# Optimization experiments

Hardware: AMD Instinct MI355X
Metric: run time of the kernel (lower is better)

Reference implementation:

```python
import jax, jax.numpy as jnp
import numpy as np

D_MODEL = 1024
N_HEADS = 16
D_K = D_MODEL // N_HEADS
B, T = 2, 2048


def setup_inputs() -> dict:
    key = jax.random.key(0)
    ks = jax.random.split(key, 9)
    s = 1.0 / np.sqrt(D_MODEL)
    def lin(kw, kb):
        W = jax.random.uniform(kw, (D_MODEL, D_MODEL), jnp.float32, -s, s)
        b = jax.random.uniform(kb, (D_MODEL,), jnp.float32, -s, s)
        return W, b
    Wq, bq = lin(ks[0], ks[1])
    Wk, bk = lin(ks[2], ks[3])
    Wv, bv = lin(ks[4], ks[5])
    Wo, bo = lin(ks[6], ks[7])
    x = jax.random.normal(ks[8], (B, T, D_MODEL), jnp.float32)
    return {"x": x, "Wq": Wq, "bq": bq, "Wk": Wk, "bk": bk,
            "Wv": Wv, "bv": bv, "Wo": Wo, "bo": bo}


def reference(x, Wq, bq, Wk, bk, Wv, bv, Wo, bo):
    Bn, Tn, _ = x.shape
    # torch Linear: x @ W.T + b
    def proj(W, b):
        y = x @ W.T + b  # [B, T, D]
        return y.reshape(Bn, Tn, N_HEADS, D_K).transpose(0, 2, 1, 3)  # [B, H, T, d_k]
    q = proj(Wq, bq)
    k = proj(Wk, bk)
    v = proj(Wv, bv)
    scores = jnp.einsum('bhqd,bhkd->bhqk', q, k) / jnp.sqrt(jnp.float32(D_K))
    causal = jnp.tril(jnp.ones((Tn, Tn), dtype=bool))  # True = keep
    scores = jnp.where(causal[None, None], scores, -jnp.inf)
    attn = jax.nn.softmax(scores, axis=-1)
    # dropout is identity in eval mode
    ctx = jnp.einsum('bhqk,bhkd->bhqd', attn, v)
    ctx = ctx.transpose(0, 2, 1, 3).reshape(Bn, Tn, D_MODEL)
    return ctx @ Wo.T + bo
```

## Files before the change

### kernel.cpp

```cpp
#include <hip/hip_runtime.h>
#include <hip/hip_bf16.h>
#include <stdint.h>

#define D_MODEL 1024
#define NH 16
#define DK 64
#define BB 2
#define TT 2048
#define NROWS (BB*TT)

#define QSCALE 0.180336880f

typedef short bf16x8 __attribute__((ext_vector_type(8)));
typedef short bf16x4 __attribute__((ext_vector_type(4)));
typedef float f32x4  __attribute__((ext_vector_type(4)));

#if __has_builtin(__builtin_amdgcn_mfma_f32_16x16x16_bf16)
  #define MFMA16(a,b,c) __builtin_amdgcn_mfma_f32_16x16x16_bf16(a,b,c,0,0,0)
  #define HAVE_M16 1
#elif __has_builtin(__builtin_amdgcn_mfma_f32_16x16x16bf16_1k)
  #define MFMA16(a,b,c) __builtin_amdgcn_mfma_f32_16x16x16bf16_1k(a,b,c,0,0,0)
  #define HAVE_M16 1
#else
  #define HAVE_M16 0
#endif

#if __has_builtin(__builtin_amdgcn_global_load_lds)
  #define HAVE_GLDS 1
__device__ __forceinline__ void gload16(const unsigned short* g, unsigned short* lds){
    __builtin_amdgcn_global_load_lds(
        (const __attribute__((address_space(1))) unsigned int*)g,
        (__attribute__((address_space(3))) unsigned int*)lds, 16, 0, 0);
}
#else
  #define HAVE_GLDS 0
#endif

__device__ __forceinline__ float fexp2(float x){
#if __has_builtin(__builtin_amdgcn_exp2f)
    return __builtin_amdgcn_exp2f(x);
#else
    return exp2f(x);
#endif
}

__device__ __forceinline__ unsigned pkbf(float a, float b){
    float2 t; t.x = a; t.y = b;
    __hip_bfloat162 h = __float22bfloat162_rn(t);
    return *reinterpret_cast<unsigned*>(&h);
}
__device__ __forceinline__ unsigned short bfbits(float a){
    __hip_bfloat16 h = __float2bfloat16(a);
    return *reinterpret_cast<unsigned short*>(&h);
}

__global__ __launch_bounds__(256) void conv_all(
    const float* __restrict__ x,
    const float* __restrict__ Wq, const float* __restrict__ Wk,
    const float* __restrict__ Wv, const float* __restrict__ Wo,
    unsigned short* __restrict__ xb, unsigned short* __restrict__ wb)
{
    const int blk = blockIdx.x;
    const float* src; unsigned short* dst; size_t i;
    if (blk < 2048) {
        src = x; dst = xb;
        i = ((size_t)blk * 256 + threadIdx.x) * 8;
    } else {
        const int t = (blk - 2048) >> 9;
        src = (t == 0) ? Wq : (t == 1) ? Wk : (t == 2) ? Wv : Wo;
        dst = wb + (size_t)t * D_MODEL * D_MODEL;
        i = ((size_t)((blk - 2048) & 511) * 256 + threadIdx.x) * 8;
    }
    float4 a = *(const float4*)(src + i);
    float4 b = *(const float4*)(src + i + 4);
    uint4 w;
    w.x = pkbf(a.x, a.y); w.y = pkbf(a.z, a.w);
    w.z = pkbf(b.x, b.y); w.w = pkbf(b.z, b.w);
    *(uint4*)(dst + i) = w;
}

__global__ __launch_bounds__(256) void conv_bf16(
    const float* __restrict__ x, unsigned short* __restrict__ y)
{
    size_t i = ((size_t)blockIdx.x * 256 + threadIdx.x) * 8;
    float4 a = *(const float4*)(x + i);
    float4 b = *(const float4*)(x + i + 4);
    uint4 w;
    w.x = pkbf(a.x, a.y); w.y = pkbf(a.z, a.w);
    w.z = pkbf(b.x, b.y); w.w = pkbf(b.z, b.w);
    *(uint4*)(y + i) = w;
}

#if HAVE_GLDS
template<int MI, int NB, bool CF32>
__device__ __forceinline__ void gemm_async(
    const unsigned short* __restrict__ Ap, const unsigned short* __restrict__ Bp,
    const float* __restrict__ bias, void* __restrict__ Cp,
    bool vt, float scale, unsigned short* As, unsigned short* Bs)
{
    constexpr int BMt = MI * 32, BNt = NB * 32;
    const int K = D_MODEL, N = D_MODEL;
    const int tid  = threadIdx.x;
    const int m0   = blockIdx.y * BMt;
    const int n0   = blockIdx.x * BNt;
    const int lane = tid & 63;
    const int w    = tid >> 6;
    const int wm   = (w >> 1) * (MI * 16);
    const int wn   = (w &  1) * (BNt / 2);
    const int l16  = lane & 15;
    const int quad = lane >> 4;
    const int crow = lane >> 2;
    const int ccol = (lane & 3) * 8;

    constexpr int CA = MI / 2;
    constexpr int CB = NB / 2;

    auto issue = [&](int buf, int k0){
        #pragma unroll
        for (int c = 0; c < CA; ++c) {
            const int chunk = w * CA + c;
            gload16(Ap + (size_t)(m0 + chunk*16 + crow) * K + k0 + ccol,
                    As + buf * BMt * 32 + chunk * 512);
        }
        #pragma unroll
        for (int c = 0; c < CB; ++c) {
            const int chunk = w * CB + c;
            gload16(Bp + (size_t)(n0 + chunk*16 + crow) * K + k0 + ccol,
                    Bs + buf * BNt * 32 + chunk * 512);
        }
    };

    f32x4 acc[MI][NB] = {};
    issue(0, 0);

    constexpr int ITER = D_MODEL / 32;
    for (int it = 0; it < ITER; ++it) {
        __syncthreads();
        if (it + 1 < ITER) issue((it + 1) & 1, (it + 1) * 32);
        const unsigned short* A = As + (it & 1) * BMt * 32;
        const unsigned short* B = Bs + (it & 1) * BNt * 32;
        bf16x8 af[MI], bg[NB];
        #pragma unroll
        for (int i = 0; i < MI; ++i)
            af[i] = *(const bf16x8*)&A[(wm + 16*i + l16) * 32 + quad * 8];
        #pragma unroll
        for (int j = 0; j < NB; ++j)
            bg[j] = *(const bf16x8*)&B[(wn + 16*j + l16) * 32 + quad * 8];
        #pragma unroll
        for (int i = 0; i < MI; ++i)
            #pragma unroll
            for (int j = 0; j < NB; ++j)
                acc[i][j] = __builtin_amdgcn_mfma_f32_16x16x32_bf16(af[i], bg[j], acc[i][j], 0, 0, 0);
    }

    #pragma unroll
    for (int j = 0; j < NB; ++j) {
        const int n = n0 + wn + 16*j + l16;
        const float bj = bias[n];
        #pragma unroll
        for (int i = 0; i < MI; ++i) {
            const int m = m0 + wm + 16*i + quad*4;
            if (vt) {
                const int b = m >> 11, t = m & 2047;
                ushort4 wv;
                wv.x = bfbits(acc[i][j][0] + bj);
                wv.y = bfbits(acc[i][j][1] + bj);
                wv.z = bfbits(acc[i][j][2] + bj);
                wv.w = bfbits(acc[i][j][3] + bj);
                *(ushort4*)((unsigned short*)Cp + (size_t)b * D_MODEL * TT
                            + (size_t)n * TT + t) = wv;
            } else {
                #pragma unroll
                for (int r = 0; r < 4; ++r) {
                    float v = (acc[i][j][r] + bj) * scale;
                    if (CF32) ((float*)Cp)[(size_t)(m + r) * N + n] = v;
                    else      ((__hip_bfloat16*)Cp)[(size_t)(m + r) * N + n] = __float2bfloat16(v);
                }
            }
        }
    }
}
#endif

#define ASTR 40

template<int MI, int NB, bool AF32, bool BF32, bool CF32>
__device__ __forceinline__ void gemm_body(
    const void* __restrict__ Ap, const void* __restrict__ Bp,
    const float* __restrict__ bias, void* __restrict__ Cp,
    bool vt, float scale, unsigned short* As, unsigned short* Bs)
{
    constexpr int BMt = MI * 32, BNt = NB * 32;
    const int K = D_MODEL, N = D_MODEL;
    const int tid  = threadIdx.x;
    const int m0   = blockIdx.y * BMt;
    const int n0   = blockIdx.x * BNt;
    const int lane = tid & 63;
    const int wave = tid >> 6;
    const int wm   = (wave >> 1) * (MI * 16);
    const int wn   = (wave &  1) * (BNt / 2);
    const int l16  = lane & 15;
    const int quad = lane >> 4;
    const int ar = (MI == 4) ? (tid >> 1) : (tid >> 2);
    const int ac = (MI == 4) ? ((tid & 1) * 16) : ((tid & 3) * 8);
    const int br = (NB == 4) ? (tid >> 1) : (tid >> 2);
    const int bc = (NB == 4) ? ((tid & 1) * 16) : ((tid & 3) * 8);

    uint4 pa[4], pb[4];

    auto loadA = [&](int k0){
        if (AF32) {
            const float* p = (const float*)Ap + (size_t)(m0 + ar) * K + k0 + ac;
            pa[0] = *(const uint4*)(p);     pa[1] = *(const uint4*)(p + 4);
            if (MI == 4) { pa[2] = *(const uint4*)(p + 8); pa[3] = *(const uint4*)(p + 12); }
        } else {
            const unsigned short* p = (const unsigned short*)Ap + (size_t)(m0 + ar) * K + k0 + ac;
            pa[0] = *(const uint4*)(p);
            if (MI == 4) pa[1] = *(const uint4*)(p + 8);
        }
    };
    auto loadB = [&](int k0){
        if (BF32) {
            const float* p = (const float*)Bp + (size_t)(n0 + br) * K + k0 + bc;
            pb[0] = *(const uint4*)(p); pb[1] = *(const uint4*)(p + 4);
            if (NB == 4) { pb[2] = *(const uint4*)(p + 8); pb[3] = *(const uint4*)(p + 12); }
        } else {
            const unsigned short* p = (const unsigned short*)Bp + (size_t)(n0 + br) * K + k0 + bc;
            pb[0] = *(const uint4*)(p);
            if (NB == 4) pb[1] = *(const uint4*)(p + 8);
        }
    };
    auto stage = [&](int buf){
        unsigned short* A = As + buf * BMt * ASTR;
        unsigned short* B = Bs + buf * BNt * ASTR;
        if (AF32) {
            const float* f = (const float*)pa;
            uint4 w0;
            w0.x = pkbf(f[0], f[1]); w0.y = pkbf(f[2], f[3]);
            w0.z = pkbf(f[4], f[5]); w0.w = pkbf(f[6], f[7]);
            *(uint4*)&A[ar*ASTR + ac] = w0;
            if (MI == 4) {
                uint4 w1;
                w1.x = pkbf(f[8], f[9]);   w1.y = pkbf(f[10], f[11]);
                w1.z = pkbf(f[12], f[13]); w1.w = pkbf(f[14], f[15]);
                *(uint4*)&A[ar*ASTR + ac + 8] = w1;
            }
        } else {
            *(uint4*)&A[ar*ASTR + ac] = pa[0];
            if (MI == 4) *(uint4*)&A[ar*ASTR + ac + 8] = pa[1];
        }
        if (BF32) {
            const float* g = (const float*)pb;
            uint4 v0;
            v0.x = pkbf(g[0], g[1]); v0.y = pkbf(g[2], g[3]);
            v0.z = pkbf(g[4], g[5]); v0.w = pkbf(g[6], g[7]);
            *(uint4*)&B[br*ASTR + bc] = v0;
            if (NB == 4) {
                uint4 v1;
                v1.x = pkbf(g[8], g[9]);   v1.y = pkbf(g[10], g[11]);
                v1.z = pkbf(g[12], g[13]); v1.w = pkbf(g[14], g[15]);
                *(uint4*)&B[br*ASTR + bc + 8] = v1;
            }
        } else {
            *(uint4*)&B[br*ASTR + bc] = pb[0];
            if (NB == 4) *(uint4*)&B[br*ASTR + bc + 8] = pb[1];
        }
    };

    f32x4 acc[MI][NB] = {};
    loadA(0); loadB(0);
    stage(0);

    constexpr int ITER = D_MODEL / 32;
    for (int it = 0; it < ITER; ++it) {
        __syncthreads();
        if (it + 1 < ITER) { loadA((it + 1) * 32); loadB((it + 1) * 32); }
        const unsigned short* A = As + (it & 1) * BMt * ASTR;
        const unsigned short* B = Bs + (it & 1) * BNt * ASTR;
        bf16x8 af[MI], bg[NB];
        #pragma unroll
        for (int i = 0; i < MI; ++i)
            af[i] = *(const bf16x8*)&A[(wm + 16*i + l16) * ASTR + quad * 8];
        #pragma unroll
        for (int j = 0; j < NB; ++j)
            bg[j] = *(const bf16x8*)&B[(wn + 16*j + l16) * ASTR + quad * 8];
        #pragma unroll
        for (int i = 0; i < MI; ++i)
            #pragma unroll
            for (int j = 0; j < NB; ++j)
                acc[i][j] = __builtin_amdgcn_mfma_f32_16x16x32_bf16(af[i], bg[j], acc[i][j], 0, 0, 0);
        if (it + 1 < ITER) stage((it + 1) & 1);
    }

    #pragma unroll
    for (int j = 0; j < NB; ++j) {
        const int n = n0 + wn + 16*j + l16;
        const float bj = bias[n];
        #pragma unroll
        for (int i = 0; i < MI; ++i) {
            const int m = m0 + wm + 16*i + quad*4;
            if (vt) {
                const int b = m >> 11, t = m & 2047;
                ushort4 wv;
                wv.x = bfbits(acc[i][j][0] + bj);
                wv.y = bfbits(acc[i][j][1] + bj);
                wv.z = bfbits(acc[i][j][2] + bj);
                wv.w = bfbits(acc[i][j][3] + bj);
                *(ushort4*)((unsigned short*)Cp + (size_t)b * D_MODEL * TT
                            + (size_t)n * TT + t) = wv;
            } else {
                #pragma unroll
                for (int r = 0; r < 4; ++r) {
                    float v = (acc[i][j][r] + bj) * scale;
                    if (CF32) ((float*)Cp)[(size_t)(m + r) * N + n] = v;
                    else      ((__hip_bfloat16*)Cp)[(size_t)(m + r) * N + n] = __float2bfloat16(v);
                }
            }
        }
    }
}

template<bool AF32, bool BF32>
__device__ __forceinline__ void qkv_sel(
    const void* x,
    const void* Wq, const float* bq, const void* Wk, const float* bk,
    const void* Wv, const float* bv,
    __hip_bfloat16* Qw, __hip_bfloat16* Kd, __hip_bfloat16* Vd,
    unsigned short* As, unsigned short* Bs)
{
    const void* W; const float* bi; void* C; bool vt = false; float sc = 1.0f;
    if      (blockIdx.z == 0) { W = Wq; bi = bq; C = Qw; sc = QSCALE; }
    else if (blockIdx.z == 1) { W = Wk; bi = bk; C = Kd; }
    else                      { W = Wv; bi = bv; C = Vd; vt = true; }
    gemm_body<4, 4, AF32, BF32, false>(x, W, bi, C, vt, sc, As, Bs);
}

#define QKV_KERNEL(name, AF, BF, XT)                                          \
__global__ __launch_bounds__(256, 3) void name(                               \
    const XT* __restrict__ x,                                                 \
    const void* __restrict__ Wq, const float* __restrict__ bq,                \
    const void* __restrict__ Wk, const float* __restrict__ bk,                \
    const void* __restrict__ Wv, const float* __restrict__ bv,                \
    __hip_bfloat16* __restrict__ Qw, __hip_bfloat16* __restrict__ Kd,         \
    __hip_bfloat16* __restrict__ Vd)                                          \
{                                                                             \
    __shared__ __align__(16) unsigned short As[2*128*ASTR];                   \
    __shared__ __align__(16) unsigned short Bs[2*128*ASTR];                   \
    qkv_sel<AF, BF>(x, Wq, bq, Wk, bk, Wv, bv, Qw, Kd, Vd, As, Bs);           \
}
QKV_KERNEL(gemm_qkv_f32, true,  true,  float)
QKV_KERNEL(gemm_qkv_xb,  false, true,  unsigned short)

__global__ __launch_bounds__(256, 3) void gemm_qkv_bb(
    const unsigned short* __restrict__ x,
    const unsigned short* __restrict__ Wq, const float* __restrict__ bq,
    const unsigned short* __restrict__ Wk, const float* __restrict__ bk,
    const unsigned short* __restrict__ Wv, const float* __restrict__ bv,
    __hip_bfloat16* __restrict__ Qw, __hip_bfloat16* __restrict__ Kd,
    __hip_bfloat16* __restrict__ Vd)
{
#if HAVE_GLDS
    __shared__ __align__(16) unsigned short As[2*128*32];
    __shared__ __align__(16) unsigned short Bs[2*128*32];
    const unsigned short* W; const float* bi; void* C; bool vt = false; float sc = 1.0f;
    if      (blockIdx.z == 0) { W = Wq; bi = bq; C = Qw; sc = QSCALE; }
    else if (blockIdx.z == 1) { W = Wk; bi = bk; C = Kd; }
    else                      { W = Wv; bi = bv; C = Vd; vt = true; }
    gemm_async<4, 4, false>(x, W, bi, C, vt, sc, As, Bs);
#else
    __shared__ __align__(16) unsigned short As[2*128*ASTR];
    __shared__ __align__(16) unsigned short Bs[2*128*ASTR];
    qkv_sel<false, false>(x, Wq, bq, Wk, bk, Wv, bv, Qw, Kd, Vd, As, Bs);
#endif
}

__global__ __launch_bounds__(256, 2) void gemm_out_f(
    const __hip_bfloat16* __restrict__ ctx, const void* __restrict__ Wo,
    const float* __restrict__ bo, float* __restrict__ out)
{
    __shared__ __align__(16) unsigned short As[2*128*ASTR];
    __shared__ __align__(16) unsigned short Bs[2*64*ASTR];
    gemm_body<4, 2, false, true, true>(ctx, Wo, bo, out, false, 1.0f, As, Bs);
}

__global__ __launch_bounds__(256, 2) void gemm_out_b(
    const __hip_bfloat16* __restrict__ ctx, const unsigned short* __restrict__ Wo,
    const float* __restrict__ bo, float* __restrict__ out)
{
#if HAVE_GLDS
    __shared__ __align__(16) unsigned short As[2*128*32];
    __shared__ __align__(16) unsigned short Bs[2*64*32];
    gemm_async<4, 2, true>((const unsigned short*)ctx, Wo, bo, out, false, 1.0f, As, Bs);
#else
    __shared__ __align__(16) unsigned short As[2*128*ASTR];
    __shared__ __align__(16) unsigned short Bs[2*64*ASTR];
    gemm_body<4, 2, false, false, true>(ctx, Wo, bo, out, false, 1.0f, As, Bs);
#endif
}

#define QSTR 68

__global__ __launch_bounds__(256, 4) void attn_mfma(
    const __hip_bfloat16* __restrict__ Q,
    const __hip_bfloat16* __restrict__ Km,
    const __hip_bfloat16* __restrict__ Vt,
    __hip_bfloat16* __restrict__ ctx)
{
    __shared__ __align__(16) unsigned short Ks [2][64*QSTR];
    __shared__ __align__(16) unsigned short VTs[2][64*QSTR];
#if !HAVE_M16
    __shared__ __align__(16) unsigned short QP[64*QSTR];
#endif

    const int tid = threadIdx.x;
    const int blk = blockIdx.x;
    const int i4 = blk & 255;
    const int j4 = blk >> 8;
    const int qt = (j4 & 1) ? (i4 & 31) : 31 - (i4 & 31);
    const int bh = (i4 >> 5) + (j4 << 3);
    const int b  = bh >> 4;
    const int h  = bh & 15;
    const int q0  = qt << 6;
    const size_t rowbase = (size_t)b * TT;
    const int colbase = h * DK;

    const int lane = tid & 63;
    const int w    = tid >> 6;
    const int l16  = lane & 15;
    const int quad = lane >> 4;
    const int lr = tid >> 2;
    const int lc = (tid & 3) << 4;

    const unsigned short* Vtb = (const unsigned short*)Vt + (size_t)b * D_MODEL * TT;

    uint4 kr0, kr1, vt0, vt1;
    auto prefetch = [&](int kv0){
        const unsigned short* pk = (const unsigned short*)Km +
            (rowbase + kv0 + lr) * D_MODEL + colbase + lc;
        kr0 = *(const uint4*)(pk);
        kr1 = *(const uint4*)(pk + 8);
        const unsigned short* pv = Vtb + (size_t)(colbase + lr) * TT + kv0 + lc;
        vt0 = *(const uint4*)(pv);
        vt1 = *(const uint4*)(pv + 8);
    };
    auto stageKV = [&](int buf){
        *(uint4*)&Ks [buf][lr*QSTR + lc]     = kr0;
        *(uint4*)&Ks [buf][lr*QSTR + lc + 8] = kr1;
        *(uint4*)&VTs[buf][lr*QSTR + lc]     = vt0;
        *(uint4*)&VTs[buf][lr*QSTR + lc + 8] = vt1;
    };

#if HAVE_M16
    const unsigned short* qp = (const unsigned short*)Q +
        (rowbase + q0 + 16*w + l16) * D_MODEL + colbase + quad*8;
    bf16x8 af_q0 = *(const bf16x8*)(qp);
    bf16x8 af_q1 = *(const bf16x8*)(qp + 32);

    prefetch(0);
    stageKV(0);

    f32x4 o[4] = {};
    float lpart = 0.0f;

    for (int kt = 0; kt <= qt; ++kt) {
        __syncthreads();
        if (kt < qt) prefetch((kt + 1) << 6);
        const int cur = kt & 1;

        f32x4 s[4] = {};
        #pragma unroll
        for (int cb = 0; cb < 4; ++cb) {
            bf16x8 ak0 = *(const bf16x8*)&Ks[cur][(16*cb + l16)*QSTR + quad*8];
            bf16x8 ak1 = *(const bf16x8*)&Ks[cur][(16*cb + l16)*QSTR + quad*8 + 32];
            s[cb] = __builtin_amdgcn_mfma_f32_16x16x32_bf16(ak0, af_q0, s[cb], 0, 0, 0);
            s[cb] = __builtin_amdgcn_mfma_f32_16x16x32_bf16(ak1, af_q1, s[cb], 0, 0, 0);
        }

        bf16x4 bp[4];
        if (kt < qt) {
            #pragma unroll
            for (int cb = 0; cb < 4; ++cb) {
                float p[4];
                #pragma unroll
                for (int r = 0; r < 4; ++r) {
                    p[r] = fexp2(fminf(s[cb][r], 36.0f));
                    lpart += p[r];
                }
                uint2 u; u.x = pkbf(p[0], p[1]); u.y = pkbf(p[2], p[3]);
                bp[cb] = *reinterpret_cast<bf16x4*>(&u);
            }
        } else {
            #pragma unroll
            for (int cb = 0; cb < 4; ++cb) {
                float p[4];
                #pragma unroll
                for (int r = 0; r < 4; ++r) {
                    float v = fminf(s[cb][r], 36.0f);
                    bool keep = (16*cb + quad*4 + r <= 16*w + l16);
                    p[r] = keep ? fexp2(v) : 0.0f;
                    lpart += p[r];
                }
                uint2 u; u.x = pkbf(p[0], p[1]); u.y = pkbf(p[2], p[3]);
                bp[cb] = *reinterpret_cast<bf16x4*>(&u);
            }
        }

        #pragma unroll
        for (int nb = 0; nb < 4; ++nb)
            #pragma unroll
            for (int cb = 0; cb < 4; ++cb) {
                bf16x4 av = *(const bf16x4*)&VTs[cur][(16*nb + l16)*QSTR + 16*cb + quad*4];
                o[nb] = MFMA16(av, bp[cb], o[nb]);
            }

        if (kt < qt) stageKV((kt + 1) & 1);
    }

    lpart += __shfl_xor(lpart, 16);
    lpart += __shfl_xor(lpart, 32);
    const float inv_l = 1.0f / lpart;

    {
        const size_t row = (rowbase + q0 + 16*w + l16) * (size_t)D_MODEL + colbase;
        #pragma unroll
        for (int nb = 0; nb < 4; ++nb) {
            ushort4 wv;
            wv.x = bfbits(o[nb][0] * inv_l);
            wv.y = bfbits(o[nb][1] * inv_l);
            wv.z = bfbits(o[nb][2] * inv_l);
            wv.w = bfbits(o[nb][3] * inv_l);
            *(ushort4*)((unsigned short*)ctx + row + 16*nb + quad*4) = wv;
        }
    }
#else
    {
        const unsigned short* p = (const unsigned short*)Q +
            (rowbase + q0 + lr) * D_MODEL + colbase + lc;
        *(uint4*)&QP[lr*QSTR + lc]     = *(const uint4*)(p);
        *(uint4*)&QP[lr*QSTR + lc + 8] = *(const uint4*)(p + 8);
    }
    prefetch(0);
    __syncthreads();
    bf16x8 af_q0 = *(const bf16x8*)&QP[(16*w + l16)*QSTR + quad*8];
    bf16x8 af_q1 = *(const bf16x8*)&QP[(16*w + l16)*QSTR + quad*8 + 32];
    stageKV(0);

    const short ob = (short)0x3F80;
    bf16x8 ones = { ob, ob, ob, ob, ob, ob, ob, ob };
    f32x4 o[4] = {};
    f32x4 l_acc = {};

    for (int kt = 0; kt <= qt; ++kt) {
        __syncthreads();
        if (kt < qt) prefetch((kt + 1) << 6);
        const int cur = kt & 1;

        f32x4 s[4] = {};
        #pragma unroll
        for (int cb = 0; cb < 4; ++cb) {
            bf16x8 bk0 = *(const bf16x8*)&Ks[cur][(16*cb + l16)*QSTR + quad*8];
            bf16x8 bk1 = *(const bf16x8*)&Ks[cur][(16*cb + l16)*QSTR + quad*8 + 32];
            s[cb] = __builtin_amdgcn_mfma_f32_16x16x32_bf16(af_q0, bk0, s[cb], 0, 0, 0);
            s[cb] = __builtin_amdgcn_mfma_f32_16x16x32_bf16(af_q1, bk1, s[cb], 0, 0, 0);
        }
        const bool diag = (kt == qt);
        #pragma unroll
        for (int cb = 0; cb < 4; ++cb)
            #pragma unroll
            for (int r = 0; r < 4; ++r) {
                float v = fminf(s[cb][r], 36.0f);
                float p = (diag && (16*cb + l16 > 16*w + quad*4 + r)) ? 0.0f : fexp2(v);
                QP[(16*w + quad*4 + r)*QSTR + 16*cb + l16] = bfbits(p);
            }
        bf16x8 ap0 = *(const bf16x8*)&QP[(16*w + l16)*QSTR + quad*8];
        bf16x8 ap1 = *(const bf16x8*)&QP[(16*w + l16)*QSTR + quad*8 + 32];
        #pragma unroll
        for (int nb = 0; nb < 4; ++nb) {
            bf16x8 bv0 = *(const bf16x8*)&VTs[cur][(16*nb + l16)*QSTR + quad*8];
            bf16x8 bv1 = *(const bf16x8*)&VTs[cur][(16*nb + l16)*QSTR + quad*8 + 32];
            o[nb] = __builtin_amdgcn_mfma_f32_16x16x32_bf16(ap0, bv0, o[nb], 0, 0, 0);
            o[nb] = __builtin_amdgcn_mfma_f32_16x16x32_bf16(ap1, bv1, o[nb], 0, 0, 0);
        }
        l_acc = __builtin_amdgcn_mfma_f32_16x16x32_bf16(ap0, ones, l_acc, 0, 0, 0);
        l_acc = __builtin_amdgcn_mfma_f32_16x16x32_bf16(ap1, ones, l_acc, 0, 0, 0);
        if (kt < qt) stageKV((kt + 1) & 1);
    }
    float inv_l[4];
    #pragma unroll
    for (int r = 0; r < 4; ++r) inv_l[r] = 1.0f / l_acc[r];
    #pragma unroll
    for (int nb = 0; nb < 4; ++nb)
        #pragma unroll
        for (int r = 0; r < 4; ++r) {
            const int row = q0 + 16*w + quad*4 + r;
            ctx[(rowbase + row)*D_MODEL + colbase + 16*nb + l16] =
                __float2bfloat16(o[nb][r] * inv_l[r]);
        }
#endif
}

extern "C" void kernel_launch(void* const* d_in, const int* in_sizes, int n_in,
                              void* d_out, int out_size, void* d_ws, size_t ws_size,
                              hipStream_t stream) {
    const float* x  = (const float*)d_in[0];
    const float* Wq = (const float*)d_in[1];
    const float* bq = (const float*)d_in[2];
    const float* Wk = (const float*)d_in[3];
    const float* bk = (const float*)d_in[4];
    const float* Wv = (const float*)d_in[5];
    const float* bv = (const float*)d_in[6];
    const float* Wo = (const float*)d_in[7];
    const float* bo = (const float*)d_in[8];

    __hip_bfloat16* Qw = (__hip_bfloat16*)d_ws;
    __hip_bfloat16* Kd = (__hip_bfloat16*)d_out;
    __hip_bfloat16* Vd = Kd + (size_t)NROWS * D_MODEL;
    unsigned short* xb = (unsigned short*)d_ws + (size_t)NROWS * D_MODEL;
    unsigned short* wb = xb + (size_t)NROWS * D_MODEL;
    const size_t WSZ = (size_t)D_MODEL * D_MODEL;

    dim3 gqkv(D_MODEL / 128, NROWS / 128, 3);
    dim3 gout(D_MODEL / 64, NROWS / 128);
    const bool haveXB = ws_size >= (size_t)(16u << 20);
    const bool haveWB = ws_size >= (size_t)(24u << 20);

    if (haveWB) {
        conv_all<<<4096, 256, 0, stream>>>(x, Wq, Wk, Wv, Wo, xb, wb);
        gemm_qkv_bb<<<gqkv, 256, 0, stream>>>(xb, wb, bq, wb + WSZ, bk,
                                              wb + 2*WSZ, bv, Qw, Kd, Vd);
    } else if (haveXB) {
        conv_bf16<<<(NROWS * D_MODEL) / (256 * 8), 256, 0, stream>>>(x, xb);
        gemm_qkv_xb<<<gqkv, 256, 0, stream>>>(xb, Wq, bq, Wk, bk, Wv, bv, Qw, Kd, Vd);
    } else {
        gemm_qkv_f32<<<gqkv, 256, 0, stream>>>(x, Wq, bq, Wk, bk, Wv, bv, Qw, Kd, Vd);
    }

    attn_mfma<<<BB * NH * (TT / 64), 256, 0, stream>>>(Qw, Kd, Vd, Qw);

    if (haveWB)
        gemm_out_b<<<gout, 256, 0, stream>>>(Qw, wb + 3*WSZ, bo, (float*)d_out);
    else
        gemm_out_f<<<gout, 256, 0, stream>>>(Qw, Wo, bo, (float*)d_out);
}
```

Measured before the change: 188.5 us.

## Pair low and high causal query tiles per attention block to share K/V loads

```diff
diff --git a/kernel.cpp b/kernel.cpp
--- a/kernel.cpp
+++ b/kernel.cpp
@@ -400,7 +400,7 @@
 
 #define QSTR 68
 
-__global__ __launch_bounds__(256, 4) void attn_mfma(
+__global__ __launch_bounds__(256, 2) void attn_mfma(
     const __hip_bfloat16* __restrict__ Q,
     const __hip_bfloat16* __restrict__ Km,
     const __hip_bfloat16* __restrict__ Vt,
@@ -416,11 +416,13 @@
     const int blk = blockIdx.x;
     const int i4 = blk & 255;
     const int j4 = blk >> 8;
-    const int qt = (j4 & 1) ? (i4 & 31) : 31 - (i4 & 31);
-    const int bh = (i4 >> 5) + (j4 << 3);
+    const int ql = (j4 & 1) ? 15 - (i4 & 15) : (i4 & 15);
+    const int qh = 31 - ql;
+    const int bh = (i4 >> 4) + (j4 << 4);
     const int b  = bh >> 4;
     const int h  = bh & 15;
-    const int q0  = qt << 6;
+    const int q0l = ql << 6;
+    const int q0h = qh << 6;
     const size_t rowbase = (size_t)b * TT;
     const int colbase = h * DK;
 
@@ -451,77 +453,104 @@
     };
 
 #if HAVE_M16
-    const unsigned short* qp = (const unsigned short*)Q +
-        (rowbase + q0 + 16*w + l16) * D_MODEL + colbase + quad*8;
-    bf16x8 af_q0 = *(const bf16x8*)(qp);
-    bf16x8 af_q1 = *(const bf16x8*)(qp + 32);
+    const unsigned short* qpl = (const unsigned short*)Q +
+        (rowbase + q0l + 16*w + l16) * D_MODEL + colbase + quad*8;
+    bf16x8 af_ql0 = *(const bf16x8*)(qpl);
+    bf16x8 af_ql1 = *(const bf16x8*)(qpl + 32);
+    const unsigned short* qph = (const unsigned short*)Q +
+        (rowbase + q0h + 16*w + l16) * D_MODEL + colbase + quad*8;
+    bf16x8 af_qh0 = *(const bf16x8*)(qph);
+    bf16x8 af_qh1 = *(const bf16x8*)(qph + 32);
 
     prefetch(0);
     stageKV(0);
 
-    f32x4 o[4] = {};
-    float lpart = 0.0f;
-
-    for (int kt = 0; kt <= qt; ++kt) {
+    f32x4 ol[4] = {}, oh[4] = {};
+    float lpl = 0.0f, lph = 0.0f;
+
+    auto softmax_t = [&](f32x4* s, bf16x4* bp, float& lp, bool diag){
+        #pragma unroll
+        for (int cb = 0; cb < 4; ++cb) {
+            float p[4];
+            #pragma unroll
+            for (int r = 0; r < 4; ++r) {
+                float v = fminf(s[cb][r], 36.0f);
+                bool keep = !diag || (16*cb + quad*4 + r <= 16*w + l16);
+                p[r] = keep ? fexp2(v) : 0.0f;
+                lp += p[r];
+            }
+            uint2 u; u.x = pkbf(p[0], p[1]); u.y = pkbf(p[2], p[3]);
+            bp[cb] = *reinterpret_cast<bf16x4*>(&u);
+        }
+    };
+
+    for (int kt = 0; kt <= ql; ++kt) {
         __syncthreads();
-        if (kt < qt) prefetch((kt + 1) << 6);
+        prefetch((kt + 1) << 6);
         const int cur = kt & 1;
 
-        f32x4 s[4] = {};
+        f32x4 sl[4] = {}, sh[4] = {};
         #pragma unroll
         for (int cb = 0; cb < 4; ++cb) {
             bf16x8 ak0 = *(const bf16x8*)&Ks[cur][(16*cb + l16)*QSTR + quad*8];
             bf16x8 ak1 = *(const bf16x8*)&Ks[cur][(16*cb + l16)*QSTR + quad*8 + 32];
-            s[cb] = __builtin_amdgcn_mfma_f32_16x16x32_bf16(ak0, af_q0, s[cb], 0, 0, 0);
-            s[cb] = __builtin_amdgcn_mfma_f32_16x16x32_bf16(ak1, af_q1, s[cb], 0, 0, 0);
-        }
-
-        bf16x4 bp[4];
-        if (kt < qt) {
-            #pragma unroll
-            for (int cb = 0; cb < 4; ++cb) {
-                float p[4];
-                #pragma unroll
-                for (int r = 0; r < 4; ++r) {
-                    p[r] = fexp2(fminf(s[cb][r], 36.0f));
-                    lpart += p[r];
-                }
-                uint2 u; u.x = pkbf(p[0], p[1]); u.y = pkbf(p[2], p[3]);
-                bp[cb] = *reinterpret_cast<bf16x4*>(&u);
-            }
-        } else {
-            #pragma unroll
-            for (int cb = 0; cb < 4; ++cb) {
-                float p[4];
-                #pragma unroll
-                for (int r = 0; r < 4; ++r) {
-                    float v = fminf(s[cb][r], 36.0f);
-                    bool keep = (16*cb + quad*4 + r <= 16*w + l16);
-                    p[r] = keep ? fexp2(v) : 0.0f;
-                    lpart += p[r];
-                }
-                uint2 u; u.x = pkbf(p[0], p[1]); u.y = pkbf(p[2], p[3]);
-                bp[cb] = *reinterpret_cast<bf16x4*>(&u);
-            }
-        }
+            sl[cb] = __builtin_amdgcn_mfma_f32_16x16x32_bf16(ak0, af_ql0, sl[cb], 0, 0, 0);
+            sl[cb] = __builtin_amdgcn_mfma_f32_16x16x32_bf16(ak1, af_ql1, sl[cb], 0, 0, 0);
+            sh[cb] = __builtin_amdgcn_mfma_f32_16x16x32_bf16(ak0, af_qh0, sh[cb], 0, 0, 0);
+            sh[cb] = __builtin_amdgcn_mfma_f32_16x16x32_bf16(ak1, af_qh1, sh[cb], 0, 0, 0);
+        }
+
+        bf16x4 bpl[4], bph[4];
+        if (kt == ql) softmax_t(sl, bpl, lpl, true);
+        else          softmax_t(sl, bpl, lpl, false);
+        softmax_t(sh, bph, lph, false);
 
         #pragma unroll
         for (int nb = 0; nb < 4; ++nb)
             #pragma unroll
             for (int cb = 0; cb < 4; ++cb) {
                 bf16x4 av = *(const bf16x4*)&VTs[cur][(16*nb + l16)*QSTR + 16*cb + quad*4];
-                o[nb] = MFMA16(av, bp[cb], o[nb]);
-            }
-
-        if (kt < qt) stageKV((kt + 1) & 1);
-    }
-
-    lpart += __shfl_xor(lpart, 16);
-    lpart += __shfl_xor(lpart, 32);
-    const float inv_l = 1.0f / lpart;
-
-    {
-        const size_t row = (rowbase + q0 + 16*w + l16) * (size_t)D_MODEL + colbase;
+                ol[nb] = MFMA16(av, bpl[cb], ol[nb]);
+                oh[nb] = MFMA16(av, bph[cb], oh[nb]);
+            }
+
+        stageKV((kt + 1) & 1);
+    }
+
+    for (int kt = ql + 1; kt <= qh; ++kt) {
+        __syncthreads();
+        if (kt < qh) prefetch((kt + 1) << 6);
+        const int cur = kt & 1;
+
+        f32x4 sh[4] = {};
+        #pragma unroll
+        for (int cb = 0; cb < 4; ++cb) {
+            bf16x8 ak0 = *(const bf16x8*)&Ks[cur][(16*cb + l16)*QSTR + quad*8];
+            bf16x8 ak1 = *(const bf16x8*)&Ks[cur][(16*cb + l16)*QSTR + quad*8 + 32];
+            sh[cb] = __builtin_amdgcn_mfma_f32_16x16x32_bf16(ak0, af_qh0, sh[cb], 0, 0, 0);
+            sh[cb] = __builtin_amdgcn_mfma_f32_16x16x32_bf16(ak1, af_qh1, sh[cb], 0, 0, 0);
+        }
+
+        bf16x4 bph[4];
+        if (kt == qh) softmax_t(sh, bph, lph, true);
+        else          softmax_t(sh, bph, lph, false);
+
+        #pragma unroll
+        for (int nb = 0; nb < 4; ++nb)
+            #pragma unroll
+            for (int cb = 0; cb < 4; ++cb) {
+                bf16x4 av = *(const bf16x4*)&VTs[cur][(16*nb + l16)*QSTR + 16*cb + quad*4];
+                oh[nb] = MFMA16(av, bph[cb], oh[nb]);
+            }
+
+        if (kt < qh) stageKV((kt + 1) & 1);
+    }
+
+    auto finish = [&](f32x4* o, float lp, int q0t){
+        lp += __shfl_xor(lp, 16);
+        lp += __shfl_xor(lp, 32);
+        const float inv_l = 1.0f / lp;
+        const size_t row = (rowbase + q0t + 16*w + l16) * (size_t)D_MODEL + colbase;
         #pragma unroll
         for (int nb = 0; nb < 4; ++nb) {
             ushort4 wv;
@@ -531,71 +560,80 @@
             wv.w = bfbits(o[nb][3] * inv_l);
             *(ushort4*)((unsigned short*)ctx + row + 16*nb + quad*4) = wv;
         }
-    }
+    };
+    finish(ol, lpl, q0l);
+    finish(oh, lph, q0h);
 #else
-    {
-        const unsigned short* p = (const unsigned short*)Q +
-            (rowbase + q0 + lr) * D_MODEL + colbase + lc;
-        *(uint4*)&QP[lr*QSTR + lc]     = *(const uint4*)(p);
-        *(uint4*)&QP[lr*QSTR + lc + 8] = *(const uint4*)(p + 8);
-    }
-    prefetch(0);
-    __syncthreads();
-    bf16x8 af_q0 = *(const bf16x8*)&QP[(16*w + l16)*QSTR + quad*8];
-    bf16x8 af_q1 = *(const bf16x8*)&QP[(16*w + l16)*QSTR + quad*8 + 32];
-    stageKV(0);
-
     const short ob = (short)0x3F80;
     bf16x8 ones = { ob, ob, ob, ob, ob, ob, ob, ob };
-    f32x4 o[4] = {};
-    f32x4 l_acc = {};
-
-    for (int kt = 0; kt <= qt; ++kt) {
+
+    for (int sel = 0; sel < 2; ++sel) {
+        const int qt = sel ? qh : ql;
+        const int q0 = qt << 6;
+
         __syncthreads();
-        if (kt < qt) prefetch((kt + 1) << 6);
-        const int cur = kt & 1;
-
-        f32x4 s[4] = {};
-        #pragma unroll
-        for (int cb = 0; cb < 4; ++cb) {
-            bf16x8 bk0 = *(const bf16x8*)&Ks[cur][(16*cb + l16)*QSTR + quad*8];
-            bf16x8 bk1 = *(const bf16x8*)&Ks[cur][(16*cb + l16)*QSTR + quad*8 + 32];
-            s[cb] = __builtin_amdgcn_mfma_f32_16x16x32_bf16(af_q0, bk0, s[cb], 0, 0, 0);
-            s[cb] = __builtin_amdgcn_mfma_f32_16x16x32_bf16(af_q1, bk1, s[cb], 0, 0, 0);
-        }
-        const bool diag = (kt == qt);
-        #pragma unroll
-        for (int cb = 0; cb < 4; ++cb)
+        {
+            const unsigned short* p = (const unsigned short*)Q +
+                (rowbase + q0 + lr) * D_MODEL + colbase + lc;
+            *(uint4*)&QP[lr*QSTR + lc]     = *(const uint4*)(p);
+            *(uint4*)&QP[lr*QSTR + lc + 8] = *(const uint4*)(p + 8);
+        }
+        prefetch(0);
+        __syncthreads();
+        bf16x8 af_q0 = *(const bf16x8*)&QP[(16*w + l16)*QSTR + quad*8];
+        bf16x8 af_q1 = *(const bf16x8*)&QP[(16*w + l16)*QSTR + quad*8 + 32];
+        stageKV(0);
+
+        f32x4 o[4] = {};
+        f32x4 l_acc = {};
+
+        for (int kt = 0; kt <= qt; ++kt) {
+            __syncthreads();
+            if (kt < qt) prefetch((kt + 1) << 6);
+            const int cur = kt & 1;
+
+            f32x4 s[4] = {};
+            #pragma unroll
+            for (int cb = 0; cb < 4; ++cb) {
+                bf16x8 bk0 = *(const bf16x8*)&Ks[cur][(16*cb + l16)*QSTR + quad*8];
+                bf16x8 bk1 = *(const bf16x8*)&Ks[cur][(16*cb + l16)*QSTR + quad*8 + 32];
+                s[cb] = __builtin_amdgcn_mfma_f32_16x16x32_bf16(af_q0, bk0, s[cb], 0, 0, 0);
+                s[cb] = __builtin_amdgcn_mfma_f32_16x16x32_bf16(af_q1, bk1, s[cb], 0, 0, 0);
+            }
+            const bool diag = (kt == qt);
+            #pragma unroll
+            for (int cb = 0; cb < 4; ++cb)
+                #pragma unroll
+                for (int r = 0; r < 4; ++r) {
+                    float v = fminf(s[cb][r], 36.0f);
+                    float p = (diag && (16*cb + l16 > 16*w + quad*4 + r)) ? 0.0f : fexp2(v);
+                    QP[(16*w + quad*4 + r)*QSTR + 16*cb + l16] = bfbits(p);
+                }
+            bf16x8 ap0 = *(const bf16x8*)&QP[(16*w + l16)*QSTR + quad*8];
+            bf16x8 ap1 = *(const bf16x8*)&QP[(16*w + l16)*QSTR + quad*8 + 32];
+            #pragma unroll
+            for (int nb = 0; nb < 4; ++nb) {
+                bf16x8 bv0 = *(const bf16x8*)&VTs[cur][(16*nb + l16)*QSTR + quad*8];
+                bf16x8 bv1 = *(const bf16x8*)&VTs[cur][(16*nb + l16)*QSTR + quad*8 + 32];
+                o[nb] = __builtin_amdgcn_mfma_f32_16x16x32_bf16(ap0, bv0, o[nb], 0, 0, 0);
+                o[nb] = __builtin_amdgcn_mfma_f32_16x16x32_bf16(ap1, bv1, o[nb], 0, 0, 0);
+            }
+            l_acc = __builtin_amdgcn_mfma_f32_16x16x32_bf16(ap0, ones, l_acc, 0, 0, 0);
+            l_acc = __builtin_amdgcn_mfma_f32_16x16x32_bf16(ap1, ones, l_acc, 0, 0, 0);
+            if (kt < qt) stageKV((kt + 1) & 1);
+        }
+        float inv_l[4];
+        #pragma unroll
+        for (int r = 0; r < 4; ++r) inv_l[r] = 1.0f / l_acc[r];
+        #pragma unroll
+        for (int nb = 0; nb < 4; ++nb)
             #pragma unroll
             for (int r = 0; r < 4; ++r) {
-                float v = fminf(s[cb][r], 36.0f);
-                float p = (diag && (16*cb + l16 > 16*w + quad*4 + r)) ? 0.0f : fexp2(v);
-                QP[(16*w + quad*4 + r)*QSTR + 16*cb + l16] = bfbits(p);
-            }
-        bf16x8 ap0 = *(const bf16x8*)&QP[(16*w + l16)*QSTR + quad*8];
-        bf16x8 ap1 = *(const bf16x8*)&QP[(16*w + l16)*QSTR + quad*8 + 32];
-        #pragma unroll
-        for (int nb = 0; nb < 4; ++nb) {
-            bf16x8 bv0 = *(const bf16x8*)&VTs[cur][(16*nb + l16)*QSTR + quad*8];
-            bf16x8 bv1 = *(const bf16x8*)&VTs[cur][(16*nb + l16)*QSTR + quad*8 + 32];
-            o[nb] = __builtin_amdgcn_mfma_f32_16x16x32_bf16(ap0, bv0, o[nb], 0, 0, 0);
-            o[nb] = __builtin_amdgcn_mfma_f32_16x16x32_bf16(ap1, bv1, o[nb], 0, 0, 0);
-        }
-        l_acc = __builtin_amdgcn_mfma_f32_16x16x32_bf16(ap0, ones, l_acc, 0, 0, 0);
-        l_acc = __builtin_amdgcn_mfma_f32_16x16x32_bf16(ap1, ones, l_acc, 0, 0, 0);
-        if (kt < qt) stageKV((kt + 1) & 1);
-    }
-    float inv_l[4];
-    #pragma unroll
-    for (int r = 0; r < 4; ++r) inv_l[r] = 1.0f / l_acc[r];
-    #pragma unroll
-    for (int nb = 0; nb < 4; ++nb)
-        #pragma unroll
-        for (int r = 0; r < 4; ++r) {
-            const int row = q0 + 16*w + quad*4 + r;
-            ctx[(rowbase + row)*D_MODEL + colbase + 16*nb + l16] =
-                __float2bfloat16(o[nb][r] * inv_l[r]);
-        }
+                const int row = q0 + 16*w + quad*4 + r;
+                ctx[(rowbase + row)*D_MODEL + colbase + 16*nb + l16] =
+                    __float2bfloat16(o[nb][r] * inv_l[r]);
+            }
+    }
 #endif
 }
 
@@ -635,7 +673,7 @@
         gemm_qkv_f32<<<gqkv, 256, 0, stream>>>(x, Wq, bq, Wk, bk, Wv, bv, Qw, Kd, Vd);
     }
 
-    attn_mfma<<<BB * NH * (TT / 64), 256, 0, stream>>>(Qw, Kd, Vd, Qw);
+    attn_mfma<<<BB * NH * (TT / 128), 256, 0, stream>>>(Qw, Kd, Vd, Qw);
 
     if (haveWB)
         gemm_out_b<<<gout, 256, 0, stream>>>(Qw, wb + 3*WSZ, bo, (float*)d_out);
```

Result: faster. 182.5 us (-3.2%).
